# Kernel tuning notes

Measured on AMD Instinct MI355X. Metric: run time of the kernel, lower is better.

The kernel has to match this reference:

```python
import jax, jax.numpy as jnp
import numpy as np

NUM_HEADS = 8
D_HEAD = 16
RY = RX = 2
PH = 2 * RY + 1
PW = 2 * RX + 1
P = PH * PW  # 25 spatial positions per patch


def setup_inputs() -> dict:
    key = jax.random.key(0)
    ks = jax.random.split(key, 7)
    B, T, H, W, C = 1, 3, 96, 96, 128
    Ck = NUM_HEADS * D_HEAD
    w = lambda k, shp: jax.random.normal(k, shp, jnp.float32) * 0.05
    return {
        "x": jax.random.normal(ks[0], (B, T, H, W, C), jnp.float32),
        "Wq": w(ks[1], (C, Ck)),
        "Wk": w(ks[2], (C, Ck)),
        "Wv": w(ks[3], (C, Ck)),
        "Wo": w(ks[4], (Ck, C)),
        "temp_emb": w(ks[5], (T, Ck)),
        "sp_emb": w(ks[6], (P, Ck)),
    }


def _neighbor_idx(N, r):
    # Edge handling: patch center is clipped into the valid interior, matching
    # extract_patches(VALID) + gather_nd with clipped indices in the original.
    c = jnp.clip(jnp.arange(N), r, N - r - 1)
    return c[:, None] + jnp.arange(-r, r + 1)[None, :]  # (N, 2r+1)


def _query_spatial_idx(H, W):
    # Position of each query pixel inside its (clipped) patch.
    yc = jnp.clip(jnp.arange(H), RY, H - RY - 1)
    xc = jnp.clip(jnp.arange(W), RX, W - RX - 1)
    yr = jnp.arange(H) - yc + RY  # (H,)
    xr = jnp.arange(W) - xc + RX  # (W,)
    return yr[:, None] * PW + xr[None, :]  # (H, W) in [0, P)


def reference(x, Wq, Wk, Wv, Wo, temp_emb, sp_emb):
    B, T, H, W, C = x.shape
    h, d = NUM_HEADS, D_HEAD
    Ck = h * d
    # 1x1 conv projections (no bias) == channel matmuls
    Q = jnp.einsum('bqyxc,ck->bqyxk', x, Wq)
    K = jnp.einsum('bqyxc,ck->bqyxk', x, Wk)
    V = jnp.einsum('bqyxc,ck->bqyxk', x, Wv)
    # positional encodings added AFTER projection (attention space)
    K = K + temp_emb[None, :, None, None, :]
    qidx = _query_spatial_idx(H, W)  # (H, W)
    Q = Q + temp_emb[None, :, None, None, :] + sp_emb[qidx][None, None]
    # local spatial patch extraction with clipped-edge handling
    ynb = _neighbor_idx(H, RY)  # (H, PH)
    xnb = _neighbor_idx(W, RX)  # (W, PW)
    Kp = K[:, :, ynb[:, None, :, None], xnb[None, :, None, :], :]  # (B,T,H,W,PH,PW,Ck)
    Vp = V[:, :, ynb[:, None, :, None], xnb[None, :, None, :], :]
    Kp = Kp.reshape(B, T, H, W, P, Ck) + sp_emb[None, None, None, None]
    Vp = Vp.reshape(B, T, H, W, P, Ck)
    # merge key time into the neighborhood axis: (B,H,W,T*P,h,d)
    Kn = Kp.transpose(0, 2, 3, 1, 4, 5).reshape(B, H, W, T * P, h, d)
    Vn = Vp.transpose(0, 2, 3, 1, 4, 5).reshape(B, H, W, T * P, h, d)
    Qh = Q.reshape(B, T, H, W, h, d)
    scale = 1.0 / jnp.sqrt(jnp.asarray(d, x.dtype))
    scores = jnp.einsum('bqyxnd,byxknd->bqyxnk', Qh, Kn) * scale
    attn = jax.nn.softmax(scores, axis=-1)  # over T*P neighborhood
    out = jnp.einsum('bqyxnk,byxknd->bqyxnd', attn, Vn).reshape(B, T, H, W, Ck)
    out = jnp.einsum('bqyxk,kc->bqyxc', out, Wo)  # output 1x1 conv
    # return_list=False -> concatenate the T outputs along channels
    return out.transpose(0, 2, 3, 1, 4).reshape(B, H, W, T * C)
```

## Files before the change

### kernel.cpp

```cpp
#include <hip/hip_runtime.h>
#include <hip/hip_bf16.h>
#include <math.h>

#define TT 3
#define HH 96
#define WWD 96
#define CCH 128
#define NROWS (TT*HH*WWD)

typedef __attribute__((ext_vector_type(8))) short short8;
typedef __attribute__((ext_vector_type(4))) short short4v;
typedef __attribute__((ext_vector_type(4))) float float4v;

__device__ __forceinline__ float bfu(unsigned short u){ union{unsigned u;float f;}c; c.u=((unsigned)u)<<16; return c.f; }
__device__ __forceinline__ unsigned short f2bf(float f){ __hip_bfloat16 h=__float2bfloat16(f); return *(unsigned short*)&h; }

#if defined(__has_builtin)
#if __has_builtin(__builtin_amdgcn_mfma_f32_16x16x16bf16_1k)
#define MFMA16(A,B,C) __builtin_amdgcn_mfma_f32_16x16x16bf16_1k(A,B,C,0,0,0)
#endif
#endif
#ifndef MFMA16
static __device__ __forceinline__ float4v mfma16_asm(short4v a, short4v b, float4v c){
    float4v d;
    asm("v_mfma_f32_16x16x16_bf16 %0, %1, %2, %3" : "=v"(d) : "v"(a), "v"(b), "v"(c));
    return d;
}
#define MFMA16(A,B,C) mfma16_asm(A,B,C)
#endif

#define QSCL 0.36067376022224085f

__launch_bounds__(256)
__global__ void prep_kernel(const float* __restrict__ Wq, const float* __restrict__ Wk,
                            const float* __restrict__ Wv, const float* __restrict__ Wo,
                            unsigned short* __restrict__ Wt, unsigned short* __restrict__ Wo1,
                            unsigned short* __restrict__ Wo2) {
    __shared__ float ts[32][33];
    const int m = blockIdx.x >> 4, tile = blockIdx.x & 15;
    const int k0 = (tile >> 2) * 32, n0 = (tile & 3) * 32;
    const float* src = (m == 0) ? Wq : (m == 1) ? Wk : (m == 2) ? Wv : Wo;
    const int tid = threadIdx.x;
    const int c = tid & 31, r8 = tid >> 5;
#pragma unroll
    for (int rr = 0; rr < 4; ++rr) {
        int r = r8 * 4 + rr;
        ts[r][c] = src[(size_t)(k0 + r) * 128 + n0 + c];
    }
    __syncthreads();
#pragma unroll
    for (int rr = 0; rr < 4; ++rr) {
        int r = r8 * 4 + rr;
        float v = ts[c][r];
        if (m < 3) {
            Wt[(size_t)(m * 128 + n0 + r) * 128 + k0 + c] = f2bf(v);
        } else {
            unsigned short w1 = f2bf(v);
            Wo1[(size_t)(n0 + r) * 128 + k0 + c] = w1;
            Wo2[(size_t)(n0 + r) * 128 + k0 + c] = f2bf(v - bfu(w1));
        }
    }
}

__launch_bounds__(256)
__global__ void qkv_kernel(const float* __restrict__ x,
                           const unsigned short* __restrict__ Wt,
                           const float* __restrict__ temp_emb,
                           const float* __restrict__ sp_emb,
                           unsigned short* __restrict__ Qb,
                           unsigned short* __restrict__ Kb,
                           unsigned short* __restrict__ Vb) {
    __shared__ unsigned short xs[32 * 136];
    const int tid = threadIdx.x;
    const int q0 = blockIdx.x * 32;
    for (int e = tid; e < 1024; e += 256) {
        int row = e >> 5, col = (e & 31) * 4;
        float4 v = *(const float4*)(x + (size_t)(q0 + row) * CCH + col);
        ushort4 u; u.x = f2bf(v.x); u.y = f2bf(v.y); u.z = f2bf(v.z); u.w = f2bf(v.w);
        *(ushort4*)&xs[row * 136 + col] = u;
    }
    __syncthreads();
    const int w = tid >> 6, lane = tid & 63, quad = lane >> 4, l16 = lane & 15;
    float4v acc[6][2];
#pragma unroll
    for (int mt = 0; mt < 6; ++mt)
#pragma unroll
        for (int nt = 0; nt < 2; ++nt) acc[mt][nt] = (float4v){0,0,0,0};
#pragma unroll
    for (int ks = 0; ks < 4; ++ks) {
        short8 b[2];
#pragma unroll
        for (int nt = 0; nt < 2; ++nt)
            b[nt] = *(const short8*)&xs[(nt * 16 + l16) * 136 + ks * 32 + quad * 8];
#pragma unroll
        for (int mt = 0; mt < 6; ++mt) {
            short8 a = *(const short8*)(Wt + (size_t)(w * 96 + mt * 16 + l16) * CCH + ks * 32 + quad * 8);
#pragma unroll
            for (int nt = 0; nt < 2; ++nt)
                acc[mt][nt] = __builtin_amdgcn_mfma_f32_16x16x32_bf16(a, b[nt], acc[mt][nt], 0, 0, 0);
        }
    }
#pragma unroll
    for (int nt = 0; nt < 2; ++nt) {
        int q = q0 + nt * 16 + l16;
        int t = q / (HH * WWD); int rem = q - t * (HH * WWD);
        int yy = rem / WWD, xx = rem - (rem / WWD) * WWD;
        int qidx = (yy - min(max(yy, 2), 93) + 2) * 5 + (xx - min(max(xx, 2), 93) + 2);
#pragma unroll
        for (int mt = 0; mt < 6; ++mt) {
            int colc = w * 96 + mt * 16 + quad * 4;
            int mat = colc >> 7, colb = colc & 127;
            float4v a = acc[mt][nt];
            ushort4 u;
            if (mat == 0) {
                float4 te = *(const float4*)(temp_emb + t * CCH + colb);
                float4 se = *(const float4*)(sp_emb + qidx * CCH + colb);
                u.x = f2bf((a[0] + te.x + se.x) * QSCL);
                u.y = f2bf((a[1] + te.y + se.y) * QSCL);
                u.z = f2bf((a[2] + te.z + se.z) * QSCL);
                u.w = f2bf((a[3] + te.w + se.w) * QSCL);
                *(ushort4*)(Qb + (size_t)q * CCH + colb) = u;
            } else if (mat == 1) {
                float4 te = *(const float4*)(temp_emb + t * CCH + colb);
                u.x = f2bf(a[0] + te.x); u.y = f2bf(a[1] + te.y);
                u.z = f2bf(a[2] + te.z); u.w = f2bf(a[3] + te.w);
                *(ushort4*)(Kb + (size_t)q * CCH + colb) = u;
            } else {
                u.x = f2bf(a[0]); u.y = f2bf(a[1]); u.z = f2bf(a[2]); u.w = f2bf(a[3]);
                *(ushort4*)(Vb + (size_t)q * CCH + colb) = u;
            }
        }
    }
}

#define PX 4
#define WIN 8

__launch_bounds__(512, 4)
__global__ void attn_kernel(const unsigned short* __restrict__ Qb,
                            const unsigned short* __restrict__ Kb,
                            const unsigned short* __restrict__ Vb,
                            const float* __restrict__ sp_emb,
                            const unsigned short* __restrict__ Wo1,
                            const unsigned short* __restrict__ Wo2,
                            float* __restrict__ out) {
    __shared__ __align__(16) char smem[75616];
    unsigned short* Ks = (unsigned short*)smem;
    unsigned short* Vt = (unsigned short*)(smem + 17408);
    float* biasL       = (float*)(smem + 34816);
    unsigned short* Os = (unsigned short*)smem;
    float* OF          = (float*)(smem + 34816);

    const int tid = threadIdx.x;
    const int lane = tid & 63;
    const int w = tid >> 6;
    const int quad = lane >> 4, l16 = lane & 15;
    const int h16 = w * 16;

    const int wg = (blockIdx.x & 7) * (576 / 8) + (blockIdx.x >> 3);
    const int bx = wg % (WWD / PX);
    const int by = wg / (WWD / PX);
    const int x0 = bx * PX, y0 = by * PX;
    const int xlo = min(max(x0 - 2, 0), WWD - WIN);
    const int ylo = min(max(y0 - 2, 0), HH - WIN);

    const int qdy = l16 >> 2, qdx = l16 & 3;
    const int yy = y0 + qdy, xx = x0 + qdx;
    const int yc = min(max(yy, 2), HH - 3), xc = min(max(xx, 2), WWD - 3);

    short4v qfr[3];
#pragma unroll
    for (int qt = 0; qt < 3; ++qt) {
        int qrow = qt * (HH * WWD) + yy * WWD + xx;
        qfr[qt] = *(const short4v*)(Qb + (size_t)qrow * CCH + h16 + quad * 4);
    }

    short4v sph[2], spl[2];
#pragma unroll
    for (int tile = 0; tile < 2; ++tile) {
        int kcr = min(tile * 16 + l16, 24);
        float4 v = *(const float4*)(sp_emb + (size_t)kcr * CCH + h16 + quad * 4);
        float vv[4] = {v.x, v.y, v.z, v.w};
        union { short4v s4; unsigned short u[4]; } ph, pl;
#pragma unroll
        for (int i = 0; i < 4; ++i) {
            ph.u[i] = f2bf(vv[i]);
            pl.u[i] = f2bf(vv[i] - bfu(ph.u[i]));
        }
        sph[tile] = ph.s4; spl[tile] = pl.s4;
    }

    const int bbase = w * (3 * 25 * 17);
#pragma unroll
    for (int qt = 0; qt < 3; ++qt) {
#pragma unroll
        for (int tile = 0; tile < 2; ++tile) {
            float4v d = MFMA16(spl[tile], qfr[qt], ((float4v){0.f,0.f,0.f,0.f}));
            d = MFMA16(sph[tile], qfr[qt], d);
#pragma unroll
            for (int r = 0; r < 4; ++r) {
                int kc = tile * 16 + quad * 4 + r;
                if (kc < 25) biasL[bbase + (qt * 25 + kc) * 17 + l16] = d[r];
            }
        }
    }

    int badr[16];
#pragma unroll
    for (int kt = 0; kt < 4; ++kt)
#pragma unroll
        for (int r = 0; r < 4; ++r) {
            int slot = kt * 16 + quad * 4 + r;
            int gy = ylo + (slot >> 3), gx = xlo + (slot & 7);
            int py = gy - yc + 2, px = gx - xc + 2;
            bool ok = (py >= 0) && (py < 5) && (px >= 0) && (px < 5);
            badr[kt * 4 + r] = ok ? (bbase + (py * 5 + px) * 17 + l16) : -1;
        }

    float m[3] = {-1e30f, -1e30f, -1e30f};
    float l[3] = {0.f, 0.f, 0.f};
    float4v oacc[3];
#pragma unroll
    for (int qt = 0; qt < 3; ++qt) oacc[qt] = (float4v){0.f,0.f,0.f,0.f};

    for (int t = 0; t < TT; ++t) {
        __syncthreads();
        for (int e = tid; e < 1024; e += 512) {
            int slot = e >> 4, c = e & 15;
            int gy = ylo + (slot >> 3), gx = xlo + (slot & 7);
            size_t g = ((size_t)(t * HH + gy) * WWD + gx) * CCH + c * 8;
            *(uint4*)&Ks[slot * 136 + c * 8] = *(const uint4*)(Kb + g);
        }
        for (int p = tid; p < 1024; p += 512) {
            int sp2 = p & 31, cq = p >> 5;
            int slot0 = sp2 * 2, ch0 = cq * 4;
            int gy = ylo + (slot0 >> 3), gx = xlo + (slot0 & 7);
            size_t g = ((size_t)(t * HH + gy) * WWD + gx) * CCH + ch0;
            uint2 a = *(const uint2*)(Vb + g);
            uint2 b = *(const uint2*)(Vb + g + CCH);
            unsigned v0 = (a.x & 0xffffu) | (b.x << 16);
            unsigned v1 = (a.x >> 16)     | (b.x & 0xffff0000u);
            unsigned v2 = (a.y & 0xffffu) | (b.y << 16);
            unsigned v3 = (a.y >> 16)     | (b.y & 0xffff0000u);
            *(unsigned*)&Vt[(ch0 + 0) * 68 + slot0] = v0;
            *(unsigned*)&Vt[(ch0 + 1) * 68 + slot0] = v1;
            *(unsigned*)&Vt[(ch0 + 2) * 68 + slot0] = v2;
            *(unsigned*)&Vt[(ch0 + 3) * 68 + slot0] = v3;
        }
        __syncthreads();

        short4v kfr[4], vfr[4];
#pragma unroll
        for (int kt = 0; kt < 4; ++kt) {
            kfr[kt] = *(const short4v*)&Ks[(kt * 16 + l16) * 136 + h16 + quad * 4];
            vfr[kt] = *(const short4v*)&Vt[(h16 + l16) * 68 + kt * 16 + quad * 4];
        }

#pragma unroll
        for (int qt = 0; qt < 3; ++qt) {
            float4v s[4];
#pragma unroll
            for (int kt = 0; kt < 4; ++kt) {
                float4v c;
#pragma unroll
                for (int r = 0; r < 4; ++r) {
                    int a = badr[kt * 4 + r];
                    c[r] = (a < 0) ? -1e30f : biasL[a + qt * 425];
                }
                s[kt] = MFMA16(kfr[kt], qfr[qt], c);
            }
            float mx = m[qt];
#pragma unroll
            for (int kt = 0; kt < 4; ++kt)
#pragma unroll
                for (int r = 0; r < 4; ++r) mx = fmaxf(mx, s[kt][r]);
            mx = fmaxf(mx, __shfl_xor(mx, 16));
            mx = fmaxf(mx, __shfl_xor(mx, 32));
            float corr = exp2f(m[qt] - mx);
            m[qt] = mx;
            l[qt] *= corr;
            float4v oc = oacc[qt] * corr;
            float lsum = 0.f;
            short4v pfr[4];
#pragma unroll
            for (int kt = 0; kt < 4; ++kt) {
                float p0 = exp2f(s[kt][0] - mx), p1 = exp2f(s[kt][1] - mx);
                float p2 = exp2f(s[kt][2] - mx), p3 = exp2f(s[kt][3] - mx);
                lsum += (p0 + p1) + (p2 + p3);
                union { short4v s4; unsigned short u[4]; } pk;
                pk.u[0] = f2bf(p0); pk.u[1] = f2bf(p1);
                pk.u[2] = f2bf(p2); pk.u[3] = f2bf(p3);
                pfr[kt] = pk.s4;
            }
            l[qt] += lsum;
#pragma unroll
            for (int kt = 0; kt < 4; ++kt) oc = MFMA16(vfr[kt], pfr[kt], oc);
            oacc[qt] = oc;
        }
    }

    __syncthreads();
#pragma unroll
    for (int qt = 0; qt < 3; ++qt) {
        float lt = l[qt];
        lt += __shfl_xor(lt, 16);
        lt += __shfl_xor(lt, 32);
        float inv = 1.f / lt;
        union { ushort4 u4; unsigned short u[4]; } ob;
#pragma unroll
        for (int r = 0; r < 4; ++r) ob.u[r] = f2bf(oacc[qt][r] * inv);
        *(ushort4*)&Os[(qt * 16 + l16) * 136 + h16 + quad * 4] = ob.u4;
    }
    __syncthreads();

    float4v pacc[3];
#pragma unroll
    for (int nt = 0; nt < 3; ++nt) pacc[nt] = (float4v){0.f, 0.f, 0.f, 0.f};
#pragma unroll
    for (int ks = 0; ks < 4; ++ks) {
        short8 bfrag[3];
#pragma unroll
        for (int nt = 0; nt < 3; ++nt)
            bfrag[nt] = *(const short8*)&Os[(nt * 16 + l16) * 136 + ks * 32 + quad * 8];
        size_t wo = (size_t)(w * 16 + l16) * CCH + ks * 32 + quad * 8;
        short8 a1 = *(const short8*)(Wo1 + wo);
        short8 a2 = *(const short8*)(Wo2 + wo);
#pragma unroll
        for (int nt = 0; nt < 3; ++nt) {
            pacc[nt] = __builtin_amdgcn_mfma_f32_16x16x32_bf16(a1, bfrag[nt], pacc[nt], 0, 0, 0);
            pacc[nt] = __builtin_amdgcn_mfma_f32_16x16x32_bf16(a2, bfrag[nt], pacc[nt], 0, 0, 0);
        }
    }
#pragma unroll
    for (int nt = 0; nt < 3; ++nt) {
        float4v a = pacc[nt];
        float4 o; o.x = a[0]; o.y = a[1]; o.z = a[2]; o.w = a[3];
        *(float4*)&OF[(nt * 16 + l16) * 132 + w * 16 + quad * 4] = o;
    }
    __syncthreads();

    for (int i = tid; i < 1536; i += 512) {
        int cy = i / 384;
        int r  = i - cy * 384;
        int row12 = r >> 5;
        int ch    = (r & 31) * 4;
        int cx = row12 / 3, nt = row12 - cx * 3;
        float4 v = *(const float4*)&OF[(nt * 16 + cy * 4 + cx) * 132 + ch];
        size_t g = ((size_t)((y0 + cy) * WWD + x0) * TT) * CCH + r * 4;
        *(float4*)(out + g) = v;
    }
}

extern "C" void kernel_launch(void* const* d_in, const int* in_sizes, int n_in,
                              void* d_out, int out_size, void* d_ws, size_t ws_size,
                              hipStream_t stream) {
    const float* x        = (const float*)d_in[0];
    const float* Wq       = (const float*)d_in[1];
    const float* Wk       = (const float*)d_in[2];
    const float* Wv       = (const float*)d_in[3];
    const float* Wo       = (const float*)d_in[4];
    const float* temp_emb = (const float*)d_in[5];
    const float* sp_emb   = (const float*)d_in[6];
    float* out = (float*)d_out;

    const size_t nb = (size_t)NROWS * CCH * 2;
    unsigned short* Qb  = (unsigned short*)d_ws;
    unsigned short* Kb  = (unsigned short*)((char*)d_ws + nb);
    unsigned short* Vb  = (unsigned short*)((char*)d_ws + 2 * nb);
    unsigned short* Wt  = (unsigned short*)((char*)d_ws + 3 * nb);
    unsigned short* Wo1 = Wt + 384 * 128;
    unsigned short* Wo2 = Wo1 + 128 * 128;

    prep_kernel<<<64, 256, 0, stream>>>(Wq, Wk, Wv, Wo, Wt, Wo1, Wo2);
    qkv_kernel<<<NROWS / 32, 256, 0, stream>>>(x, Wt, temp_emb, sp_emb, Qb, Kb, Vb);
    attn_kernel<<<(HH / PX) * (WWD / PX), 512, 0, stream>>>(Qb, Kb, Vb, sp_emb, Wo1, Wo2, out);
}
```

Measured before the change: 149.4 us.

## Stage QKV projection outputs through LDS for coalesced row-wise stores

The QKV projection kernel now handles 64 rows per block with 512 threads, and each wave computes a 16-column slice of Q, K and V instead of 96 mixed columns. Accumulators are written into an LDS buffer (reusing the input tile memory) and read back row-major, so each thread stores contiguous 8-byte chunks along a row. This is meant to replace the scattered strided bf16 stores and per-element mat branching with coalesced writes and uniform per-matrix epilogues. The cost is three extra LDS round trips and six block barriers, plus a larger block that may reduce occupancy.

```diff
diff --git a/kernel.cpp b/kernel.cpp
--- a/kernel.cpp
+++ b/kernel.cpp
@@ -62,7 +62,7 @@
     }
 }
 
-__launch_bounds__(256)
+__launch_bounds__(512)
 __global__ void qkv_kernel(const float* __restrict__ x,
                            const unsigned short* __restrict__ Wt,
                            const float* __restrict__ temp_emb,
@@ -70,65 +70,80 @@
                            unsigned short* __restrict__ Qb,
                            unsigned short* __restrict__ Kb,
                            unsigned short* __restrict__ Vb) {
-    __shared__ unsigned short xs[32 * 136];
+    __shared__ __align__(16) char smem[33792];
+    unsigned short* xs = (unsigned short*)smem;
+    float* OF          = (float*)smem;
+
     const int tid = threadIdx.x;
-    const int q0 = blockIdx.x * 32;
-    for (int e = tid; e < 1024; e += 256) {
+    const int q0 = blockIdx.x * 64;
+    const int t = q0 / (HH * WWD);
+
+    for (int e = tid; e < 2048; e += 512) {
         int row = e >> 5, col = (e & 31) * 4;
         float4 v = *(const float4*)(x + (size_t)(q0 + row) * CCH + col);
         ushort4 u; u.x = f2bf(v.x); u.y = f2bf(v.y); u.z = f2bf(v.z); u.w = f2bf(v.w);
         *(ushort4*)&xs[row * 136 + col] = u;
     }
     __syncthreads();
+
     const int w = tid >> 6, lane = tid & 63, quad = lane >> 4, l16 = lane & 15;
-    float4v acc[6][2];
-#pragma unroll
-    for (int mt = 0; mt < 6; ++mt)
-#pragma unroll
-        for (int nt = 0; nt < 2; ++nt) acc[mt][nt] = (float4v){0,0,0,0};
+
+    float4v acc[3][4];
+#pragma unroll
+    for (int m = 0; m < 3; ++m)
+#pragma unroll
+        for (int nt = 0; nt < 4; ++nt) acc[m][nt] = (float4v){0,0,0,0};
+
 #pragma unroll
     for (int ks = 0; ks < 4; ++ks) {
-        short8 b[2];
-#pragma unroll
-        for (int nt = 0; nt < 2; ++nt)
+        short8 b[4];
+#pragma unroll
+        for (int nt = 0; nt < 4; ++nt)
             b[nt] = *(const short8*)&xs[(nt * 16 + l16) * 136 + ks * 32 + quad * 8];
 #pragma unroll
-        for (int mt = 0; mt < 6; ++mt) {
-            short8 a = *(const short8*)(Wt + (size_t)(w * 96 + mt * 16 + l16) * CCH + ks * 32 + quad * 8);
-#pragma unroll
-            for (int nt = 0; nt < 2; ++nt)
-                acc[mt][nt] = __builtin_amdgcn_mfma_f32_16x16x32_bf16(a, b[nt], acc[mt][nt], 0, 0, 0);
-        }
-    }
-#pragma unroll
-    for (int nt = 0; nt < 2; ++nt) {
-        int q = q0 + nt * 16 + l16;
-        int t = q / (HH * WWD); int rem = q - t * (HH * WWD);
-        int yy = rem / WWD, xx = rem - (rem / WWD) * WWD;
-        int qidx = (yy - min(max(yy, 2), 93) + 2) * 5 + (xx - min(max(xx, 2), 93) + 2);
-#pragma unroll
-        for (int mt = 0; mt < 6; ++mt) {
-            int colc = w * 96 + mt * 16 + quad * 4;
-            int mat = colc >> 7, colb = colc & 127;
-            float4v a = acc[mt][nt];
+        for (int m = 0; m < 3; ++m) {
+            short8 a = *(const short8*)(Wt + (size_t)(m * 128 + w * 16 + l16) * CCH + ks * 32 + quad * 8);
+#pragma unroll
+            for (int nt = 0; nt < 4; ++nt)
+                acc[m][nt] = __builtin_amdgcn_mfma_f32_16x16x32_bf16(a, b[nt], acc[m][nt], 0, 0, 0);
+        }
+    }
+
+    unsigned short* dst[3] = {Qb, Kb, Vb};
+#pragma unroll
+    for (int m = 0; m < 3; ++m) {
+        __syncthreads();
+#pragma unroll
+        for (int nt = 0; nt < 4; ++nt) {
+            float4v a = acc[m][nt];
+            float4 o; o.x = a[0]; o.y = a[1]; o.z = a[2]; o.w = a[3];
+            *(float4*)&OF[(nt * 16 + l16) * 132 + w * 16 + quad * 4] = o;
+        }
+        __syncthreads();
+        for (int e = tid; e < 2048; e += 512) {
+            int row = e >> 5, c4 = (e & 31);
+            int ch = c4 * 4;
+            float4 v = *(const float4*)&OF[row * 132 + ch];
+            int q = q0 + row;
             ushort4 u;
-            if (mat == 0) {
-                float4 te = *(const float4*)(temp_emb + t * CCH + colb);
-                float4 se = *(const float4*)(sp_emb + qidx * CCH + colb);
-                u.x = f2bf((a[0] + te.x + se.x) * QSCL);
-                u.y = f2bf((a[1] + te.y + se.y) * QSCL);
-                u.z = f2bf((a[2] + te.z + se.z) * QSCL);
-                u.w = f2bf((a[3] + te.w + se.w) * QSCL);
-                *(ushort4*)(Qb + (size_t)q * CCH + colb) = u;
-            } else if (mat == 1) {
-                float4 te = *(const float4*)(temp_emb + t * CCH + colb);
-                u.x = f2bf(a[0] + te.x); u.y = f2bf(a[1] + te.y);
-                u.z = f2bf(a[2] + te.z); u.w = f2bf(a[3] + te.w);
-                *(ushort4*)(Kb + (size_t)q * CCH + colb) = u;
+            if (m == 0) {
+                int rem = q - t * (HH * WWD);
+                int yy = rem / WWD, xx = rem - (rem / WWD) * WWD;
+                int qidx = (yy - min(max(yy, 2), 93) + 2) * 5 + (xx - min(max(xx, 2), 93) + 2);
+                float4 te = *(const float4*)(temp_emb + t * CCH + ch);
+                float4 se = *(const float4*)(sp_emb + qidx * CCH + ch);
+                u.x = f2bf((v.x + te.x + se.x) * QSCL);
+                u.y = f2bf((v.y + te.y + se.y) * QSCL);
+                u.z = f2bf((v.z + te.z + se.z) * QSCL);
+                u.w = f2bf((v.w + te.w + se.w) * QSCL);
+            } else if (m == 1) {
+                float4 te = *(const float4*)(temp_emb + t * CCH + ch);
+                u.x = f2bf(v.x + te.x); u.y = f2bf(v.y + te.y);
+                u.z = f2bf(v.z + te.z); u.w = f2bf(v.w + te.w);
             } else {
-                u.x = f2bf(a[0]); u.y = f2bf(a[1]); u.z = f2bf(a[2]); u.w = f2bf(a[3]);
-                *(ushort4*)(Vb + (size_t)q * CCH + colb) = u;
+                u.x = f2bf(v.x); u.y = f2bf(v.y); u.z = f2bf(v.z); u.w = f2bf(v.w);
             }
+            *(ushort4*)(dst[m] + (size_t)q * CCH + ch) = u;
         }
     }
 }
@@ -372,6 +387,6 @@
     unsigned short* Wo2 = Wo1 + 128 * 128;
 
     prep_kernel<<<64, 256, 0, stream>>>(Wq, Wk, Wv, Wo, Wt, Wo1, Wo2);
-    qkv_kernel<<<NROWS / 32, 256, 0, stream>>>(x, Wt, temp_emb, sp_emb, Qb, Kb, Vb);
+    qkv_kernel<<<NROWS / 64, 512, 0, stream>>>(x, Wt, temp_emb, sp_emb, Qb, Kb, Vb);
     attn_kernel<<<(HH / PX) * (WWD / PX), 512, 0, stream>>>(Qb, Kb, Vb, sp_emb, Wo1, Wo2, out);
 }
```

Result: faster. 131.2 us, median of 3 (-12.2%).
